# Kernel tuning notes

Measured on AMD Instinct MI355X. Metric: run time of the kernel, lower is better.

Reference implementation:

```python
import jax, jax.numpy as jnp
import numpy as np

N_NODES = 100000
N_EDGES = 1600000
IN_CH = 256
OUT_CH = 128
EPS = 1e-12


def setup_inputs() -> dict:
    key = jax.random.key(0)
    k1, k2, k3 = jax.random.split(key, 3)
    x = jax.random.normal(k1, (N_NODES, IN_CH), dtype=jnp.float32)
    edge_index = jax.random.randint(k2, (2, N_EDGES), 0, N_NODES, dtype=jnp.int64)
    W = jax.random.normal(k3, (IN_CH, OUT_CH), dtype=jnp.float32) / np.float32(np.sqrt(IN_CH))
    b = jnp.zeros((OUT_CH,), dtype=jnp.float32)
    return {"x": x, "edge_index": edge_index, "W": W, "b": b}


def reference(x, edge_index, W, b):
    n = x.shape[0]
    # GCNConv: linear transform first, then normalized aggregation with self-loops
    h = x @ W  # [N, out]
    loops = jnp.arange(n, dtype=edge_index.dtype)
    row = jnp.concatenate([edge_index[0], loops])  # source nodes
    col = jnp.concatenate([edge_index[1], loops])  # destination nodes
    deg = jax.ops.segment_sum(jnp.ones_like(col, dtype=h.dtype), col, num_segments=n)
    dinv = jnp.where(deg > 0, jax.lax.rsqrt(jnp.maximum(deg, 1.0)), 0.0)  # deg^-1/2, inf->0
    wgt = dinv[row] * dinv[col]  # symmetric normalization per edge
    agg = jax.ops.segment_sum(h[row] * wgt[:, None], col, num_segments=n) + b  # [N, out]
    # min-max scale per node (dim=1)
    zmin = agg.min(axis=1, keepdims=True)
    zmax = agg.max(axis=1, keepdims=True)
    z = (agg - zmin) / (zmax - zmin)
    # F.normalize: L2 along dim=1 with eps clamp
    nrm = jnp.maximum(jnp.linalg.norm(z, axis=1, keepdims=True), EPS)
    return z / nrm
```

## Files before the change

### kernel.cpp

```cpp
#include <hip/hip_runtime.h>
#include <hip/hip_bf16.h>

#define N_NODES 100000
#define N_EDGES 1600000
#define IN_CH 256
#define OUT_CH 128

#define BSZ 256
#define NBUCK 391
#define BCAP 4736
#define CSC 4096

#define GEMM_ROWS 32

typedef __attribute__((ext_vector_type(8))) short short8;
typedef __attribute__((ext_vector_type(4))) float floatx4;
typedef __attribute__((ext_vector_type(2))) float float2v;

union bfu { __hip_bfloat16 b; unsigned short u; };

__device__ inline unsigned short f2bf(float v) {
    bfu cv; cv.b = __float2bfloat16(v); return cv.u;
}
__device__ inline float bf2f(unsigned short u) {
    bfu cv; cv.u = u; return __bfloat162float(cv.b);
}

__device__ inline void pkacc(float2v& acc, unsigned g) {
    float2v v;
    v.x = __uint_as_float(g << 16);
    v.y = __uint_as_float(g & 0xffff0000u);
    asm("v_pk_add_f32 %0, %1, %2" : "=v"(acc) : "v"(v), "v"(acc));
}

__global__ void k_prep_w(const float* __restrict__ W,
                         unsigned short* __restrict__ wb_hi,
                         unsigned short* __restrict__ wb_lo,
                         int* __restrict__ bcursor,
                         unsigned* __restrict__ zrow) {
    int tid = threadIdx.x;
    if (blockIdx.x == 0) {
        if (tid < NBUCK) bcursor[tid] = 0;
        if (tid + 256 < NBUCK) bcursor[tid + 256] = 0;
    }
    if (blockIdx.x == 1 && tid < 64) zrow[tid] = 0;

    int t = blockIdx.x * 256 + tid;
    if (t >= IN_CH * OUT_CH) return;
    int j = t & 7;
    int lane = (t >> 3) & 63;
    int s = (t >> 9) & 7;
    int nt = t >> 12;
    int k = s * 32 + (lane >> 4) * 8 + j;
    int n = nt * 16 + (lane & 15);
    float w = W[k * OUT_CH + n];
    unsigned short hi = f2bf(w);
    wb_hi[t] = hi;
    wb_lo[t] = f2bf(w - bf2f(hi));
}

__global__ __launch_bounds__(512) void pa_scatter(const int* __restrict__ rows,
                                                  const int* __restrict__ cols,
                                                  int* __restrict__ bcursor,
                                                  unsigned* __restrict__ ebuf) {
    __shared__ int lcnt[NBUCK];
    __shared__ int lbase[NBUCK];
    int t = threadIdx.x;
    if (t < NBUCK) lcnt[t] = 0;
    __syncthreads();
    int s0 = blockIdx.x * CSC;
    int e1 = min(N_EDGES, s0 + CSC);
    for (int i = s0 + t; i < e1; i += 512) atomicAdd(&lcnt[cols[i] >> 8], 1);
    __syncthreads();
    if (t < NBUCK) {
        int c = lcnt[t];
        lbase[t] = c ? atomicAdd(&bcursor[t], c) : 0;
        lcnt[t] = 0;
    }
    __syncthreads();
    for (int i = s0 + t; i < e1; i += 512) {
        int c = cols[i], r = rows[i];
        int bk = c >> 8;
        int rank = atomicAdd(&lcnt[bk], 1);
        ebuf[bk * BCAP + lbase[bk] + rank] = ((unsigned)(c & (BSZ - 1)) << 17) | (unsigned)r;
    }
}

__global__ __launch_bounds__(512) void pb_build(const unsigned* __restrict__ ebuf,
                                                const int* __restrict__ bcursor,
                                                int* __restrict__ cnt,
                                                int* __restrict__ base,
                                                float* __restrict__ dinv,
                                                int* __restrict__ es) {
    __shared__ int nh[BSZ];
    __shared__ int sc[BSZ];
    __shared__ int lcur[BSZ];
    int t = threadIdx.x;
    int bk = blockIdx.x;
    int bb = bk * BCAP;
    int bc = bcursor[bk];
    if (t < BSZ) { nh[t] = 0; lcur[t] = 0; }
    __syncthreads();
    for (int i = t; i < bc; i += 512) atomicAdd(&nh[ebuf[bb + i] >> 17], 1);
    __syncthreads();
    if (t < BSZ) sc[t] = nh[t];
    __syncthreads();
    for (int off = 1; off < BSZ; off <<= 1) {
        int v = (t < BSZ && t >= off) ? sc[t - off] : 0;
        __syncthreads();
        if (t < BSZ) sc[t] += v;
        __syncthreads();
    }
    if (t < BSZ) {
        int node = bk * BSZ + t;
        if (node < N_NODES) {
            int c = nh[t];
            cnt[node] = c;
            base[node] = bb + sc[t] - c;
            dinv[node] = rsqrtf((float)(c + 1));
        }
    }
    for (int i = t; i < bc; i += 512) {
        unsigned v = ebuf[bb + i];
        int dl = v >> 17;
        int src = (int)(v & 0x1FFFFu);
        int rank = atomicAdd(&lcur[dl], 1);
        es[bb + sc[dl] - nh[dl] + rank] = src << 8;
    }
}

__global__ __launch_bounds__(512) void k_gemm(const float* __restrict__ x,
                                              const unsigned short* __restrict__ wb_hi,
                                              const unsigned short* __restrict__ wb_lo,
                                              const float* __restrict__ dinv,
                                              unsigned short* __restrict__ hbs) {
    __shared__ short8 xbh[2 * 8 * 68];
    __shared__ short8 xbl[2 * 8 * 68];
    int t = threadIdx.x;
    int wv = t >> 6;
    int lane = t & 63;
    int row0 = blockIdx.x * GEMM_ROWS;

    short8 Bh[8], Bl[8];
    const short8* bhp = (const short8*)wb_hi + (size_t)wv * 8 * 64 + lane;
    const short8* blp = (const short8*)wb_lo + (size_t)wv * 8 * 64 + lane;
#pragma unroll
    for (int s = 0; s < 8; ++s) {
        Bh[s] = bhp[s * 64];
        Bl[s] = blp[s * 64];
    }

#pragma unroll
    for (int q = 0; q < 2; ++q) {
        int c = q * 512 + t;
        int row = c >> 5;
        int cc  = c & 31;
        const float4* xp = (const float4*)(x + (size_t)(row0 + row) * IN_CH + cc * 8);
        float4 v0 = xp[0];
        float4 v1 = xp[1];
        float xv[8] = {v0.x, v0.y, v0.z, v0.w, v1.x, v1.y, v1.z, v1.w};
        short8 hh, ll;
#pragma unroll
        for (int j = 0; j < 8; ++j) {
            unsigned short hi = f2bf(xv[j]);
            hh[j] = (short)hi;
            ll[j] = (short)f2bf(xv[j] - bf2f(hi));
        }
        int ms = row >> 4, r15 = row & 15, s = cc >> 2, q2 = cc & 3;
        int idx = (ms * 8 + s) * 68 + q2 * 17 + r15;
        xbh[idx] = hh;
        xbl[idx] = ll;
    }
    __syncthreads();

    int r15 = lane & 15;
    int quad = lane >> 4;
    int lidx = quad * 17 + r15;

    floatx4 acc[2];
#pragma unroll
    for (int ms = 0; ms < 2; ++ms) {
        acc[ms] = (floatx4){0.f, 0.f, 0.f, 0.f};
#pragma unroll
        for (int s = 0; s < 8; ++s) {
            short8 ah = xbh[(ms * 8 + s) * 68 + lidx];
            short8 al = xbl[(ms * 8 + s) * 68 + lidx];
            acc[ms] = __builtin_amdgcn_mfma_f32_16x16x32_bf16(ah, Bh[s], acc[ms], 0, 0, 0);
            acc[ms] = __builtin_amdgcn_mfma_f32_16x16x32_bf16(ah, Bl[s], acc[ms], 0, 0, 0);
            acc[ms] = __builtin_amdgcn_mfma_f32_16x16x32_bf16(al, Bh[s], acc[ms], 0, 0, 0);
        }
    }

#pragma unroll
    for (int ms = 0; ms < 2; ++ms)
#pragma unroll
        for (int r = 0; r < 4; ++r) {
            int row = row0 + ms * 16 + quad * 4 + r;
            size_t idx = (size_t)row * OUT_CH + wv * 16 + r15;
            hbs[idx] = f2bf(acc[ms][r] * dinv[row]);
        }
}

__global__ __launch_bounds__(256) void k_agg_fin(const unsigned short* __restrict__ hbs,
                                                 const float* __restrict__ dinv,
                                                 const int* __restrict__ es,
                                                 const int* __restrict__ base,
                                                 const int* __restrict__ cnt,
                                                 const float* __restrict__ b,
                                                 float* __restrict__ out) {
    int t = threadIdx.x;
    int lane = t & 63;
    int ll = lane & 15;
    int node = blockIdx.x * 16 + (t >> 4);

    const char* hb = (const char*)hbs;
    int lane_byte = ll << 4;
    int bidx = (lane & 48) << 2;

    float dn = dinv[node];
    int d  = cnt[node];
    int st = base[node];

    float4 bv0 = ((const float4*)b)[ll * 2];
    float4 bv1 = ((const float4*)b)[ll * 2 + 1];

    uint4 gs = *(const uint4*)(hb + ((size_t)node << 8) + lane_byte);
    float2v acc[4];
    acc[0].x = __uint_as_float(gs.x << 16); acc[0].y = __uint_as_float(gs.x & 0xffff0000u);
    acc[1].x = __uint_as_float(gs.y << 16); acc[1].y = __uint_as_float(gs.y & 0xffff0000u);
    acc[2].x = __uint_as_float(gs.z << 16); acc[2].y = __uint_as_float(gs.z & 0xffff0000u);
    acc[3].x = __uint_as_float(gs.w << 16); acc[3].y = __uint_as_float(gs.w & 0xffff0000u);

    int dm = d;
    dm = max(dm, __shfl_xor(dm, 16, 64));
    dm = max(dm, __shfl_xor(dm, 32, 64));
    int iters = __builtin_amdgcn_readfirstlane((dm + 15) >> 4);

    const int zoff = N_NODES << 8;

    for (int it = 0; it < iters; ++it) {
        int jb = it << 4;
        int off = zoff;
        if (jb + ll < d) off = es[st + jb + ll];

        uint4 ga[4], gb[4];
#pragma unroll
        for (int k = 0; k < 4; ++k) {
            int ro = __builtin_amdgcn_ds_bpermute(bidx + (k << 2), off);
            ga[k] = *(const uint4*)(hb + (unsigned)(ro + lane_byte));
        }
#pragma unroll
        for (int k = 0; k < 4; ++k) {
            int ro = __builtin_amdgcn_ds_bpermute(bidx + ((4 + k) << 2), off);
            gb[k] = *(const uint4*)(hb + (unsigned)(ro + lane_byte));
        }
#pragma unroll
        for (int k = 0; k < 4; ++k) {
            pkacc(acc[0], ga[k].x); pkacc(acc[1], ga[k].y);
            pkacc(acc[2], ga[k].z); pkacc(acc[3], ga[k].w);
        }
#pragma unroll
        for (int k = 0; k < 4; ++k) {
            int ro = __builtin_amdgcn_ds_bpermute(bidx + ((8 + k) << 2), off);
            ga[k] = *(const uint4*)(hb + (unsigned)(ro + lane_byte));
        }
#pragma unroll
        for (int k = 0; k < 4; ++k) {
            pkacc(acc[0], gb[k].x); pkacc(acc[1], gb[k].y);
            pkacc(acc[2], gb[k].z); pkacc(acc[3], gb[k].w);
        }
#pragma unroll
        for (int k = 0; k < 4; ++k) {
            int ro = __builtin_amdgcn_ds_bpermute(bidx + ((12 + k) << 2), off);
            gb[k] = *(const uint4*)(hb + (unsigned)(ro + lane_byte));
        }
#pragma unroll
        for (int k = 0; k < 4; ++k) {
            pkacc(acc[0], ga[k].x); pkacc(acc[1], ga[k].y);
            pkacc(acc[2], ga[k].z); pkacc(acc[3], ga[k].w);
        }
#pragma unroll
        for (int k = 0; k < 4; ++k) {
            pkacc(acc[0], gb[k].x); pkacc(acc[1], gb[k].y);
            pkacc(acc[2], gb[k].z); pkacc(acc[3], gb[k].w);
        }
    }

    float v[8];
    v[0] = dn * acc[0].x + bv0.x;  v[1] = dn * acc[0].y + bv0.y;
    v[2] = dn * acc[1].x + bv0.z;  v[3] = dn * acc[1].y + bv0.w;
    v[4] = dn * acc[2].x + bv1.x;  v[5] = dn * acc[2].y + bv1.y;
    v[6] = dn * acc[3].x + bv1.z;  v[7] = dn * acc[3].y + bv1.w;

    float lmin = v[0], lmax = v[0];
#pragma unroll
    for (int i = 1; i < 8; ++i) { lmin = fminf(lmin, v[i]); lmax = fmaxf(lmax, v[i]); }
#pragma unroll
    for (int m = 8; m; m >>= 1) {
        lmin = fminf(lmin, __shfl_xor(lmin, m, 64));
        lmax = fmaxf(lmax, __shfl_xor(lmax, m, 64));
    }
    float scale = 1.0f / (lmax - lmin);
    float z[8];
    float ss = 0.f;
#pragma unroll
    for (int i = 0; i < 8; ++i) { z[i] = (v[i] - lmin) * scale; ss += z[i] * z[i]; }
#pragma unroll
    for (int m = 8; m; m >>= 1) ss += __shfl_xor(ss, m, 64);
    float inv = 1.0f / fmaxf(sqrtf(ss), 1e-12f);

    float4 o0 = {z[0] * inv, z[1] * inv, z[2] * inv, z[3] * inv};
    float4 o1 = {z[4] * inv, z[5] * inv, z[6] * inv, z[7] * inv};
    float4* op = (float4*)(out + (size_t)node * OUT_CH);
    op[ll * 2] = o0;
    op[ll * 2 + 1] = o1;
}

extern "C" void kernel_launch(void* const* d_in, const int* in_sizes, int n_in,
                              void* d_out, int out_size, void* d_ws, size_t ws_size,
                              hipStream_t stream) {
    const float* x = (const float*)d_in[0];
    const int* ei = (const int*)d_in[1];
    const float* W = (const float*)d_in[2];
    const float* b = (const float*)d_in[3];
    float* out = (float*)d_out;

    char* ws = (char*)d_ws;
    size_t o = 0;
    auto alloc = [&](size_t bytes) { void* p = ws + o; o = (o + bytes + 255) & ~(size_t)255; return p; };
    float* dinv    = (float*)alloc((size_t)N_NODES * 4);
    int*   cnt     = (int*)  alloc((size_t)N_NODES * 4);
    int*   base    = (int*)  alloc((size_t)N_NODES * 4);
    int*   bcursor = (int*)  alloc(NBUCK * 4);
    unsigned short* wb_hi = (unsigned short*)alloc((size_t)IN_CH * OUT_CH * 2);
    unsigned short* wb_lo = (unsigned short*)alloc((size_t)IN_CH * OUT_CH * 2);
    unsigned short* hbs = (unsigned short*)alloc((size_t)(N_NODES + 1) * OUT_CH * 2);
    unsigned* ebuf = (unsigned*)alloc((size_t)NBUCK * BCAP * 4);
    int*   es      = (int*)  alloc((size_t)NBUCK * BCAP * 4);

    const int* rows = ei;
    const int* cols = ei + N_EDGES;

    k_prep_w<<<(IN_CH * OUT_CH + 255) / 256, 256, 0, stream>>>(
        W, wb_hi, wb_lo, bcursor, (unsigned*)(hbs + (size_t)N_NODES * OUT_CH));

    pa_scatter<<<(N_EDGES + CSC - 1) / CSC, 512, 0, stream>>>(rows, cols, bcursor, ebuf);
    pb_build<<<NBUCK, 512, 0, stream>>>(ebuf, bcursor, cnt, base, dinv, es);

    k_gemm<<<N_NODES / GEMM_ROWS, 512, 0, stream>>>(x, wb_hi, wb_lo, dinv, hbs);

    k_agg_fin<<<N_NODES / 16, 256, 0, stream>>>(hbs, dinv, es, base, cnt, b, out);
}
```

Before: 284.2 us.

## Fuse weight prep into scatter, register-cache edge ranks, double GEMM tile rows

The weight hi/lo split now runs in extra blocks of the edge-scatter kernel, and the bucket-cursor and zero-row clears become hipMemsetAsync calls, removing one kernel launch. The scatter and build kernels keep the edge values and their atomic ranks in registers from the counting pass, so they skip a second global read and a second round of shared atomics. The GEMM now handles 64 rows per block, with bounds guards, to amortize each wave's B-fragment loads over more rows. The trade-offs are higher register and LDS use per block, a fixed 10-iteration unroll in pb_build that assumes no bucket holds more than 5120 edges, and two extra memset operations.

```diff
diff --git a/kernel.cpp b/kernel.cpp
--- a/kernel.cpp
+++ b/kernel.cpp
@@ -10,8 +10,10 @@
 #define NBUCK 391
 #define BCAP 4736
 #define CSC 4096
-
-#define GEMM_ROWS 32
+#define SCB 391
+#define PREPB 64
+
+#define GEMM_ROWS 64
 
 typedef __attribute__((ext_vector_type(8))) short short8;
 typedef __attribute__((ext_vector_type(4))) float floatx4;
@@ -33,56 +35,60 @@
     asm("v_pk_add_f32 %0, %1, %2" : "=v"(acc) : "v"(v), "v"(acc));
 }
 
-__global__ void k_prep_w(const float* __restrict__ W,
-                         unsigned short* __restrict__ wb_hi,
-                         unsigned short* __restrict__ wb_lo,
-                         int* __restrict__ bcursor,
-                         unsigned* __restrict__ zrow) {
-    int tid = threadIdx.x;
-    if (blockIdx.x == 0) {
-        if (tid < NBUCK) bcursor[tid] = 0;
-        if (tid + 256 < NBUCK) bcursor[tid + 256] = 0;
-    }
-    if (blockIdx.x == 1 && tid < 64) zrow[tid] = 0;
-
-    int t = blockIdx.x * 256 + tid;
-    if (t >= IN_CH * OUT_CH) return;
-    int j = t & 7;
-    int lane = (t >> 3) & 63;
-    int s = (t >> 9) & 7;
-    int nt = t >> 12;
-    int k = s * 32 + (lane >> 4) * 8 + j;
-    int n = nt * 16 + (lane & 15);
-    float w = W[k * OUT_CH + n];
-    unsigned short hi = f2bf(w);
-    wb_hi[t] = hi;
-    wb_lo[t] = f2bf(w - bf2f(hi));
-}
-
-__global__ __launch_bounds__(512) void pa_scatter(const int* __restrict__ rows,
-                                                  const int* __restrict__ cols,
-                                                  int* __restrict__ bcursor,
-                                                  unsigned* __restrict__ ebuf) {
+__global__ __launch_bounds__(512) void k_scatter_prep(const int* __restrict__ rows,
+                                                      const int* __restrict__ cols,
+                                                      int* __restrict__ bcursor,
+                                                      unsigned* __restrict__ ebuf,
+                                                      const float* __restrict__ W,
+                                                      unsigned short* __restrict__ wb_hi,
+                                                      unsigned short* __restrict__ wb_lo) {
+    if (blockIdx.x >= SCB) {
+        int t = (blockIdx.x - SCB) * 512 + threadIdx.x;
+        int j = t & 7;
+        int lane = (t >> 3) & 63;
+        int s = (t >> 9) & 7;
+        int nt = t >> 12;
+        int k = s * 32 + (lane >> 4) * 8 + j;
+        int n = nt * 16 + (lane & 15);
+        float w = W[k * OUT_CH + n];
+        unsigned short hi = f2bf(w);
+        wb_hi[t] = hi;
+        wb_lo[t] = f2bf(w - bf2f(hi));
+        return;
+    }
+
     __shared__ int lcnt[NBUCK];
     __shared__ int lbase[NBUCK];
     int t = threadIdx.x;
-    if (t < NBUCK) lcnt[t] = 0;
-    __syncthreads();
+    for (int i = t; i < NBUCK; i += 512) lcnt[i] = 0;
+    __syncthreads();
+
     int s0 = blockIdx.x * CSC;
     int e1 = min(N_EDGES, s0 + CSC);
-    for (int i = s0 + t; i < e1; i += 512) atomicAdd(&lcnt[cols[i] >> 8], 1);
-    __syncthreads();
-    if (t < NBUCK) {
-        int c = lcnt[t];
-        lbase[t] = c ? atomicAdd(&bcursor[t], c) : 0;
-        lcnt[t] = 0;
-    }
-    __syncthreads();
-    for (int i = s0 + t; i < e1; i += 512) {
-        int c = cols[i], r = rows[i];
+
+    unsigned val[8];
+    int bkr[8], rk[8];
+#pragma unroll
+    for (int u = 0; u < 8; ++u) {
+        int i = s0 + t + u * 512;
+        bool p = i < e1;
+        int c = p ? cols[i] : 0;
+        int r = p ? rows[i] : 0;
         int bk = c >> 8;
-        int rank = atomicAdd(&lcnt[bk], 1);
-        ebuf[bk * BCAP + lbase[bk] + rank] = ((unsigned)(c & (BSZ - 1)) << 17) | (unsigned)r;
+        bkr[u] = bk;
+        val[u] = ((unsigned)(c & (BSZ - 1)) << 17) | (unsigned)r;
+        rk[u] = p ? atomicAdd(&lcnt[bk], 1) : 0;
+    }
+    __syncthreads();
+    for (int i = t; i < NBUCK; i += 512) {
+        int c = lcnt[i];
+        lbase[i] = c ? atomicAdd(&bcursor[i], c) : 0;
+    }
+    __syncthreads();
+#pragma unroll
+    for (int u = 0; u < 8; ++u) {
+        int i = s0 + t + u * 512;
+        if (i < e1) ebuf[bkr[u] * BCAP + lbase[bkr[u]] + rk[u]] = val[u];
     }
 }
 
@@ -94,14 +100,23 @@
                                                 int* __restrict__ es) {
     __shared__ int nh[BSZ];
     __shared__ int sc[BSZ];
-    __shared__ int lcur[BSZ];
     int t = threadIdx.x;
     int bk = blockIdx.x;
     int bb = bk * BCAP;
     int bc = bcursor[bk];
-    if (t < BSZ) { nh[t] = 0; lcur[t] = 0; }
-    __syncthreads();
-    for (int i = t; i < bc; i += 512) atomicAdd(&nh[ebuf[bb + i] >> 17], 1);
+    if (t < BSZ) nh[t] = 0;
+    __syncthreads();
+
+    unsigned val[10];
+    int rk[10];
+#pragma unroll
+    for (int u = 0; u < 10; ++u) {
+        int i = t + u * 512;
+        bool p = i < bc;
+        unsigned v = p ? ebuf[bb + i] : 0u;
+        val[u] = v;
+        rk[u] = p ? atomicAdd(&nh[v >> 17], 1) : 0;
+    }
     __syncthreads();
     if (t < BSZ) sc[t] = nh[t];
     __syncthreads();
@@ -120,12 +135,14 @@
             dinv[node] = rsqrtf((float)(c + 1));
         }
     }
-    for (int i = t; i < bc; i += 512) {
-        unsigned v = ebuf[bb + i];
-        int dl = v >> 17;
-        int src = (int)(v & 0x1FFFFu);
-        int rank = atomicAdd(&lcur[dl], 1);
-        es[bb + sc[dl] - nh[dl] + rank] = src << 8;
+#pragma unroll
+    for (int u = 0; u < 10; ++u) {
+        int i = t + u * 512;
+        if (i < bc) {
+            unsigned v = val[u];
+            int dl = v >> 17;
+            es[bb + sc[dl] - nh[dl] + rk[u]] = (int)(v & 0x1FFFFu) << 8;
+        }
     }
 }
 
@@ -134,8 +151,8 @@
                                               const unsigned short* __restrict__ wb_lo,
                                               const float* __restrict__ dinv,
                                               unsigned short* __restrict__ hbs) {
-    __shared__ short8 xbh[2 * 8 * 68];
-    __shared__ short8 xbl[2 * 8 * 68];
+    __shared__ short8 xbh[4 * 8 * 68];
+    __shared__ short8 xbl[4 * 8 * 68];
     int t = threadIdx.x;
     int wv = t >> 6;
     int lane = t & 63;
@@ -151,11 +168,12 @@
     }
 
 #pragma unroll
-    for (int q = 0; q < 2; ++q) {
+    for (int q = 0; q < 4; ++q) {
         int c = q * 512 + t;
         int row = c >> 5;
         int cc  = c & 31;
-        const float4* xp = (const float4*)(x + (size_t)(row0 + row) * IN_CH + cc * 8);
+        int gr = min(row0 + row, N_NODES - 1);
+        const float4* xp = (const float4*)(x + (size_t)gr * IN_CH + cc * 8);
         float4 v0 = xp[0];
         float4 v1 = xp[1];
         float xv[8] = {v0.x, v0.y, v0.z, v0.w, v1.x, v1.y, v1.z, v1.w};
@@ -177,9 +195,9 @@
     int quad = lane >> 4;
     int lidx = quad * 17 + r15;
 
-    floatx4 acc[2];
-#pragma unroll
-    for (int ms = 0; ms < 2; ++ms) {
+    floatx4 acc[4];
+#pragma unroll
+    for (int ms = 0; ms < 4; ++ms) {
         acc[ms] = (floatx4){0.f, 0.f, 0.f, 0.f};
 #pragma unroll
         for (int s = 0; s < 8; ++s) {
@@ -192,12 +210,14 @@
     }
 
 #pragma unroll
-    for (int ms = 0; ms < 2; ++ms)
+    for (int ms = 0; ms < 4; ++ms)
 #pragma unroll
         for (int r = 0; r < 4; ++r) {
             int row = row0 + ms * 16 + quad * 4 + r;
-            size_t idx = (size_t)row * OUT_CH + wv * 16 + r15;
-            hbs[idx] = f2bf(acc[ms][r] * dinv[row]);
+            if (row < N_NODES) {
+                size_t idx = (size_t)row * OUT_CH + wv * 16 + r15;
+                hbs[idx] = f2bf(acc[ms][r] * dinv[row]);
+            }
         }
 }
 
@@ -341,13 +361,16 @@
     const int* rows = ei;
     const int* cols = ei + N_EDGES;
 
-    k_prep_w<<<(IN_CH * OUT_CH + 255) / 256, 256, 0, stream>>>(
-        W, wb_hi, wb_lo, bcursor, (unsigned*)(hbs + (size_t)N_NODES * OUT_CH));
-
-    pa_scatter<<<(N_EDGES + CSC - 1) / CSC, 512, 0, stream>>>(rows, cols, bcursor, ebuf);
+    hipMemsetAsync(bcursor, 0, NBUCK * sizeof(int), stream);
+    hipMemsetAsync(hbs + (size_t)N_NODES * OUT_CH, 0, OUT_CH * 2, stream);
+
+    k_scatter_prep<<<SCB + PREPB, 512, 0, stream>>>(rows, cols, bcursor, ebuf,
+                                                    W, wb_hi, wb_lo);
+
     pb_build<<<NBUCK, 512, 0, stream>>>(ebuf, bcursor, cnt, base, dinv, es);
 
-    k_gemm<<<N_NODES / GEMM_ROWS, 512, 0, stream>>>(x, wb_hi, wb_lo, dinv, hbs);
+    k_gemm<<<(N_NODES + GEMM_ROWS - 1) / GEMM_ROWS, 512, 0, stream>>>(
+        x, wb_hi, wb_lo, dinv, hbs);
 
     k_agg_fin<<<N_NODES / 16, 256, 0, stream>>>(hbs, dinv, es, base, cnt, b, out);
 }
```

New measurement: 290.4 us. 2.2% more time.
